# Kernel optimization log

Measured on AMD Instinct MI355X. Metric: run time of the kernel, lower is better.

Reference implementation:

```python
import jax, jax.numpy as jnp
import numpy as np

N_NODES = 100000
N_EDGES = 600000
IN_CH = 128
HID = 64
N_REL = 8


def setup_inputs() -> dict:
    key = jax.random.key(0)
    ks = jax.random.split(key, 9)
    x = jax.random.normal(ks[0], (N_NODES, IN_CH), dtype=jnp.float32)
    edge_index = jax.random.randint(ks[1], (2, N_EDGES), 0, N_NODES)
    edge_type = jax.random.randint(ks[2], (N_EDGES,), 0, N_REL)
    s_in = 1.0 / np.sqrt(IN_CH)   # torch Linear init bound
    s_h = 1.0 / np.sqrt(HID)
    W_rel = jax.random.uniform(ks[3], (N_REL, HID, IN_CH), minval=-s_in, maxval=s_in, dtype=jnp.float32)
    b_rel = jax.random.uniform(ks[4], (N_REL, HID), minval=-s_in, maxval=s_in, dtype=jnp.float32)
    W_self = jax.random.uniform(ks[5], (HID, IN_CH), minval=-s_in, maxval=s_in, dtype=jnp.float32)
    b_self = jax.random.uniform(ks[6], (HID,), minval=-s_in, maxval=s_in, dtype=jnp.float32)
    W_out = jax.random.uniform(ks[7], (1, HID), minval=-s_h, maxval=s_h, dtype=jnp.float32)
    b_out = jax.random.uniform(ks[8], (1,), minval=-s_h, maxval=s_h, dtype=jnp.float32)
    return {"x": x, "edge_index": edge_index, "edge_type": edge_type,
            "W_rel": W_rel, "b_rel": b_rel, "W_self": W_self, "b_self": b_self,
            "W_out": W_out, "b_out": b_out}


def reference(x, edge_index, edge_type, W_rel, b_rel, W_self, b_self, W_out, b_out):
    row, col = edge_index[0], edge_index[1]
    R, H, _ = W_rel.shape
    N = x.shape[0]
    # Project every node under every relation once ([R, N, H]) instead of the
    # per-relation masked gather->GEMM loop: same math (sum over edges of
    # W_{edge_type} x_{src} + b_{edge_type} scattered into dst).
    xp = jnp.einsum('ni,rhi->rnh', x, W_rel)                     # [R, N, H]
    msg = xp.reshape(R * N, H)[edge_type * N + row] + b_rel[edge_type]  # [E, H]
    agg = jax.ops.segment_sum(msg, col, num_segments=N)          # scatter-add into dst
    out = jax.nn.relu(agg + x @ W_self.T + b_self)               # [N, H]
    return (out @ W_out.T + b_out)[:, 0]                          # [N]
```

## Files before the change

kernel.cpp:

```cpp
#include <hip/hip_runtime.h>
#include <hip/hip_bf16.h>

#define IN_CH    128
#define HID      64
#define N_REL    8
#define ZCH      576
#define SLOT_CAP 32
#define NBKT     784
#define BKT_CAP  1024
#define ZBLK     128

using bf16x8 = __attribute__((ext_vector_type(8))) short;
using f32x4  = __attribute__((ext_vector_type(4))) float;

__device__ __forceinline__ short f2bf(float f) {
    unsigned int u = __float_as_uint(f);
    u += 0x7fffu + ((u >> 16) & 1u);
    return (short)(u >> 16);
}

__global__ __launch_bounds__(1024) void prep0_kernel(
    const float* __restrict__ W_rel, const float* __restrict__ W_self,
    unsigned short* __restrict__ wpk2, unsigned int* __restrict__ gcount)
{
    const int b = blockIdx.x, tid = threadIdx.x;
    if (b < 9) {
        int gid  = b * 1024 + tid;
        int kt   = gid / 2304;
        int rem  = gid - kt * 2304;
        int mt   = rem >> 6;
        int lane = rem & 63;
        int ch   = mt * 16 + (lane & 15);
        int k0   = kt * 32 + ((lane >> 4) << 3);
        bf16x8 o;
        #pragma unroll
        for (int j = 0; j < 8; ++j) {
            int k = k0 + j;
            float v = (ch < 512)
                ? W_rel[(size_t)(ch >> 6) * (HID * IN_CH) + (size_t)(ch & 63) * IN_CH + k]
                : W_self[(size_t)(ch - 512) * IN_CH + k];
            o[j] = f2bf(v);
        }
        *(bf16x8*)(wpk2 + (size_t)gid * 8) = o;
    } else {
        if (tid < NBKT) gcount[tid] = 0u;
    }
}

__global__ __launch_bounds__(1024) void k1_kernel(
    const int* __restrict__ edge_index, const int* __restrict__ edge_type,
    unsigned int* __restrict__ gcount, uint2* __restrict__ gbuf, int E, int nbB,
    const float* __restrict__ x, const unsigned short* __restrict__ wpk2,
    unsigned short* __restrict__ z, int N)
{
    __shared__ unsigned int hist[NBKT];
    __shared__ short xs[ZBLK * 136];
    const int b = blockIdx.x, tid = threadIdx.x;
    if (b < nbB) {
        for (int i = tid; i < NBKT; i += 1024) hist[i] = 0u;
        __syncthreads();
        const int e0 = (b * 1024 + tid) * 8;
        unsigned int pay[8]; unsigned int dstv[8]; unsigned int rnk[8]; int bkt[8];
        const bool full = (e0 + 8 <= E);
        if (full) {
            int4 s0 = *(const int4*)(edge_index + e0);
            int4 s1 = *(const int4*)(edge_index + e0 + 4);
            int4 d0 = *(const int4*)(edge_index + E + e0);
            int4 d1 = *(const int4*)(edge_index + E + e0 + 4);
            int4 t0 = *(const int4*)(edge_type + e0);
            int4 t1 = *(const int4*)(edge_type + e0 + 4);
            const int* sp0 = &s0.x; const int* sp1 = &s1.x;
            const int* dp0 = &d0.x; const int* dp1 = &d1.x;
            const int* tp0 = &t0.x; const int* tp1 = &t1.x;
            #pragma unroll
            for (int j = 0; j < 4; ++j) {
                pay[j]     = (unsigned int)sp0[j] * 1152u
                           + ((unsigned int)tp0[j] << 7) + ((unsigned int)tp0[j] << 28);
                dstv[j]    = (unsigned int)dp0[j];
                pay[j + 4] = (unsigned int)sp1[j] * 1152u
                           + ((unsigned int)tp1[j] << 7) + ((unsigned int)tp1[j] << 28);
                dstv[j + 4]= (unsigned int)dp1[j];
            }
            #pragma unroll
            for (int j = 0; j < 8; ++j) {
                bkt[j] = (int)(dstv[j] >> 7);
                rnk[j] = atomicAdd(&hist[bkt[j]], 1u);
            }
        }
        __syncthreads();
        for (int bb = tid; bb < NBKT; bb += 1024) {
            unsigned int c = hist[bb];
            if (c) hist[bb] = atomicAdd(&gcount[bb], c);
        }
        __syncthreads();
        if (full) {
            #pragma unroll
            for (int j = 0; j < 8; ++j) {
                unsigned int p = hist[bkt[j]] + rnk[j];
                if (p < BKT_CAP) {
                    uint2 v; v.x = pay[j]; v.y = dstv[j];
                    gbuf[(size_t)bkt[j] * BKT_CAP + p] = v;
                }
            }
        }
    } else {
        const int nodebase = (b - nbB) * ZBLK;
        {
            int node = tid >> 3;
            int ch0  = (tid & 7) * 16;
            int ng   = nodebase + node;
            if (ng < N) {
                const float* p = x + (size_t)ng * IN_CH + ch0;
                float4 a0 = *(const float4*)p;
                float4 a1 = *(const float4*)(p + 4);
                float4 a2 = *(const float4*)(p + 8);
                float4 a3 = *(const float4*)(p + 12);
                bf16x8 o0, o1;
                o0[0]=f2bf(a0.x); o0[1]=f2bf(a0.y); o0[2]=f2bf(a0.z); o0[3]=f2bf(a0.w);
                o0[4]=f2bf(a1.x); o0[5]=f2bf(a1.y); o0[6]=f2bf(a1.z); o0[7]=f2bf(a1.w);
                o1[0]=f2bf(a2.x); o1[1]=f2bf(a2.y); o1[2]=f2bf(a2.z); o1[3]=f2bf(a2.w);
                o1[4]=f2bf(a3.x); o1[5]=f2bf(a3.y); o1[6]=f2bf(a3.z); o1[7]=f2bf(a3.w);
                *(bf16x8*)(xs + node * 136 + ch0)     = o0;
                *(bf16x8*)(xs + node * 136 + ch0 + 8) = o1;
            }
        }
        __syncthreads();
        const int wave = tid >> 6, lane = tid & 63;
        const int nt   = wave >> 1;
        const int mt0  = (wave & 1) * 18;
        const short* abase = xs + (nt * 16 + (lane & 15)) * 136 + ((lane >> 4) << 3);
        const bf16x8* wv = (const bf16x8*)wpk2;
        const int nbase = nodebase + nt * 16 + ((lane >> 4) << 2);
        for (int mti = 0; mti < 18; ++mti) {
            const int mt = mt0 + mti;
            f32x4 acc = {0.f, 0.f, 0.f, 0.f};
            #pragma unroll
            for (int kt = 0; kt < 4; ++kt) {
                bf16x8 a  = *(const bf16x8*)(abase + kt * 32);
                bf16x8 bb = wv[(size_t)((kt * 36 + mt) * 64) + lane];
                acc = __builtin_amdgcn_mfma_f32_16x16x32_bf16(a, bb, acc, 0, 0, 0);
            }
            const int ch = mt * 16 + (lane & 15);
            #pragma unroll
            for (int j = 0; j < 4; ++j) {
                int n = nbase + j;
                if (n < N)
                    z[(size_t)n * ZCH + ch] = (unsigned short)f2bf(acc[j]);
            }
        }
    }
}

__global__ __launch_bounds__(256) void k2_kernel(
    const unsigned int* __restrict__ gcount, const uint2* __restrict__ gbuf,
    int* __restrict__ cnt, unsigned int* __restrict__ slots, int N)
{
    __shared__ unsigned int hist[128];
    const int b = blockIdx.x, tid = threadIdx.x;
    if (tid < 128) hist[tid] = 0u;
    __syncthreads();
    unsigned int bc = gcount[b]; if (bc > BKT_CAP) bc = BKT_CAP;
    for (unsigned int i = tid; i < bc; i += 256) {
        uint2 v = gbuf[(size_t)b * BKT_CAP + i];
        unsigned int d = v.y;
        unsigned int r = atomicAdd(&hist[d & 127], 1u);
        if (r < SLOT_CAP) slots[(size_t)d * SLOT_CAP + r] = v.x;
    }
    __syncthreads();
    if (tid < 128) {
        int d = b * 128 + tid;
        if (d < N) cnt[d] = (int)hist[tid];
    }
}

__global__ __launch_bounds__(256) void agg_kernel(
    const unsigned short* __restrict__ z, const int* __restrict__ cnt,
    const unsigned int* __restrict__ slots,
    const float* __restrict__ b_rel, const float* __restrict__ b_self,
    const float* __restrict__ W_out, const float* __restrict__ b_out,
    float* __restrict__ out, int N)
{
    const int tid  = threadIdx.x;
    const int g    = blockIdx.x * 4 + (tid >> 6);
    const int lane = tid & 63;

    const int rawdeg = cnt[g];
    unsigned int ev = 0u;
    if (lane < SLOT_CAP) ev = slots[(size_t)g * SLOT_CAP + lane];
    const float selfv =
        __uint_as_float((unsigned int)z[(size_t)g * ZCH + 512 + lane] << 16);

    const int deg = (rawdeg > SLOT_CAP) ? SLOT_CAP : rawdeg;
    const int myr = (lane < deg) ? (int)(ev >> 28) : 8;
    int cr[8];
    #pragma unroll
    for (int r = 0; r < 8; ++r) cr[r] = (int)__popcll(__ballot(myr == r));

    const char* zb = (const char*)z;
    float agg = 0.f;
    for (int e0 = 0; e0 < deg; e0 += 8) {
        int bn = deg - e0; if (bn > 8) bn = 8;
        unsigned int sv[8]; unsigned short gv[8];
        #pragma unroll
        for (int i = 0; i < 8; ++i) {
            if (i < bn) {
                sv[i] = (unsigned int)__builtin_amdgcn_readlane((int)ev, e0 + i);
                gv[i] = *(const unsigned short*)(zb + (sv[i] & 0x0FFFFFFFu) + (lane << 1));
            }
        }
        #pragma unroll
        for (int i = 0; i < 8; ++i) {
            if (i >= bn) break;
            agg += __uint_as_float((unsigned int)gv[i] << 16);
        }
    }

    float h = agg + selfv + b_self[lane];
    #pragma unroll
    for (int r = 0; r < 8; ++r)
        h += (float)cr[r] * b_rel[r * HID + lane];
    h = fmaxf(h, 0.f) * W_out[lane];
    #pragma unroll
    for (int m = 32; m >= 1; m >>= 1)
        h += __shfl_xor(h, m, 64);
    if (lane == 0) out[g] = h + b_out[0];
}

extern "C" void kernel_launch(void* const* d_in, const int* in_sizes, int n_in,
                              void* d_out, int out_size, void* d_ws, size_t ws_size,
                              hipStream_t stream)
{
    const float* x          = (const float*)d_in[0];
    const int*   edge_index = (const int*)  d_in[1];
    const int*   edge_type  = (const int*)  d_in[2];
    const float* W_rel      = (const float*)d_in[3];
    const float* b_rel      = (const float*)d_in[4];
    const float* W_self     = (const float*)d_in[5];
    const float* b_self     = (const float*)d_in[6];
    const float* W_out      = (const float*)d_in[7];
    const float* b_out      = (const float*)d_in[8];
    float* out = (float*)d_out;

    const int N = in_sizes[0] / IN_CH;
    const int E = in_sizes[2];

    char* w = (char*)d_ws;
    unsigned short* wpk2 = (unsigned short*)w; w += 147456;
    int* cnt             = (int*)w;            w += ((size_t)N * 4 + 255) & ~255ull;
    unsigned int* slots  = (unsigned int*)w;   w += (size_t)N * SLOT_CAP * 4;
    unsigned int* gcount = (unsigned int*)w;   w += (NBKT * 4 + 255) & ~255;
    uint2* gbuf          = (uint2*)w;          w += (size_t)NBKT * BKT_CAP * 8;
    unsigned short* z    = (unsigned short*)w; w += (size_t)N * ZCH * 2;

    const int nbB     = (E + 8191) / 8192;
    const int zblocks = (N + ZBLK - 1) / ZBLK;

    prep0_kernel<<<10, 1024, 0, stream>>>(W_rel, W_self, wpk2, gcount);

    k1_kernel<<<nbB + zblocks, 1024, 0, stream>>>(
        edge_index, edge_type, gcount, gbuf, E, nbB, x, wpk2, z, N);

    k2_kernel<<<NBKT, 256, 0, stream>>>(gcount, gbuf, cnt, slots, N);

    agg_kernel<<<N / 4, 256, 0, stream>>>(
        z, cnt, slots, b_rel, b_self, W_out, b_out, out, N);
}
```

Baseline: 228.8 us.

## Swap MFMA operands to keep weight fragments in registers and pack z stores

The node-projection GEMM now gives each wave a fixed output-channel tile, holds its four weight fragments in registers and loops over the eight node tiles. Swapping the MFMA A and B operands makes each lane own four consecutive channels of one node, so the results are written as one 8-byte packed store instead of four scattered 2-byte stores. The aim is to cut repeated global weight loads and uncoalesced z writes. Work per wave now depends on a 16-wave block (36 channel tiles spread over 3 reps), so some waves get less work than others.

```diff
diff --git a/kernel.cpp b/kernel.cpp
--- a/kernel.cpp
+++ b/kernel.cpp
@@ -126,26 +126,35 @@
         }
         __syncthreads();
         const int wave = tid >> 6, lane = tid & 63;
-        const int nt   = wave >> 1;
-        const int mt0  = (wave & 1) * 18;
-        const short* abase = xs + (nt * 16 + (lane & 15)) * 136 + ((lane >> 4) << 3);
         const bf16x8* wv = (const bf16x8*)wpk2;
-        const int nbase = nodebase + nt * 16 + ((lane >> 4) << 2);
-        for (int mti = 0; mti < 18; ++mti) {
-            const int mt = mt0 + mti;
-            f32x4 acc = {0.f, 0.f, 0.f, 0.f};
-            #pragma unroll
-            for (int kt = 0; kt < 4; ++kt) {
-                bf16x8 a  = *(const bf16x8*)(abase + kt * 32);
-                bf16x8 bb = wv[(size_t)((kt * 36 + mt) * 64) + lane];
-                acc = __builtin_amdgcn_mfma_f32_16x16x32_bf16(a, bb, acc, 0, 0, 0);
-            }
-            const int ch = mt * 16 + (lane & 15);
-            #pragma unroll
-            for (int j = 0; j < 4; ++j) {
-                int n = nbase + j;
-                if (n < N)
-                    z[(size_t)n * ZCH + ch] = (unsigned short)f2bf(acc[j]);
+        const short* abase0 = xs + (lane & 15) * 136 + ((lane >> 4) << 3);
+        #pragma unroll
+        for (int rep = 0; rep < 3; ++rep) {
+            const int mt = rep * 16 + wave;
+            if (mt >= 36) break;
+            bf16x8 wfrag[4];
+            #pragma unroll
+            for (int kt = 0; kt < 4; ++kt)
+                wfrag[kt] = wv[(size_t)((kt * 36 + mt) * 64) + lane];
+            const int ch0 = mt * 16 + ((lane >> 4) << 2);
+            for (int nt = 0; nt < 8; ++nt) {
+                const short* abase = abase0 + nt * 16 * 136;
+                f32x4 acc = {0.f, 0.f, 0.f, 0.f};
+                #pragma unroll
+                for (int kt = 0; kt < 4; ++kt) {
+                    bf16x8 a = *(const bf16x8*)(abase + kt * 32);
+                    acc = __builtin_amdgcn_mfma_f32_16x16x32_bf16(
+                        wfrag[kt], a, acc, 0, 0, 0);
+                }
+                const int n = nodebase + nt * 16 + (lane & 15);
+                if (n < N) {
+                    uint2 v;
+                    v.x = ((unsigned int)(unsigned short)f2bf(acc[1]) << 16)
+                        | (unsigned int)(unsigned short)f2bf(acc[0]);
+                    v.y = ((unsigned int)(unsigned short)f2bf(acc[3]) << 16)
+                        | (unsigned int)(unsigned short)f2bf(acc[2]);
+                    *(uint2*)(z + (size_t)n * ZCH + ch0) = v;
+                }
             }
         }
     }
```

New measurement: 258.8 us. 13.1% more time.
